# Kernel tuning notes

Hardware: AMD Instinct MI355X
Metric: run time of the kernel (lower is better)

## Reference

```python
import jax, jax.numpy as jnp
import numpy as np

N_NODES = 10000
N_EDGES = 160000
D = 128        # embedding_dim = in/out channels
E_DIM = 32     # edge feature dim
HEADS = 3
N_ETYPES = 64
ROUNDS = 2     # num_message_rounds
NEG_SLOPE = 0.2


def _lookup_maxnorm(table, idx):
    # torch Embedding(max_norm=1): rows with L2 norm > 1 are renormalized to norm 1
    v = table[idx]
    n = jnp.linalg.norm(v, axis=-1, keepdims=True)
    return v / jnp.maximum(n, 1.0)


def _edge_gat(x, src, dst, edge_attr, weight, att, euw, bias):
    # x: [N, D]; src/dst: [E] (self loops included); edge_attr: [E, E_DIM]
    N = x.shape[0]
    H = HEADS
    C = weight.shape[1] // H
    xh = (x @ weight).reshape(N, H, C)                 # [N, H, C]
    x_j = xh[src]                                      # gather source nodes  [E, H, C]
    x_i = xh[dst]                                      # gather target nodes  [E, H, C]
    ea = jnp.broadcast_to(edge_attr[:, None, :], (src.shape[0], H, edge_attr.shape[-1]))
    xj_cat = jnp.concatenate([x_j, ea], axis=-1)       # [E, H, C+E_DIM]
    # attention logits: (cat(x_i, x_j, e) * att).sum(-1)
    alpha = jnp.sum(jnp.concatenate([x_i, xj_cat], axis=-1) * att, axis=-1)  # [E, H]
    alpha = jax.nn.leaky_relu(alpha, NEG_SLOPE)
    # scatter-softmax over incoming edges of each dst node (stable)
    m = jax.ops.segment_max(alpha, dst, num_segments=N)        # [N, H]
    a = jnp.exp(alpha - m[dst])
    denom = jax.ops.segment_sum(a, dst, num_segments=N)        # [N, H]
    a = a / denom[dst]
    # weighted scatter-add aggregate
    aggr = jax.ops.segment_sum(xj_cat * a[..., None], dst, num_segments=N)  # [N, H, C+E_DIM]
    return aggr.mean(axis=1) @ euw + bias                       # [N, C]


def setup_inputs() -> dict:
    key = jax.random.key(0)
    ks = jax.random.split(key, 13)
    x_idx = jnp.arange(N_NODES, dtype=jnp.int32)
    src = jax.random.randint(ks[0], (N_EDGES,), 0, N_NODES, dtype=jnp.int32)
    off = jax.random.randint(ks[1], (N_EDGES,), 1, N_NODES, dtype=jnp.int32)
    dst = (src + off) % N_NODES    # guaranteed self-loop-free
    edge_index = jnp.stack([src, dst])
    edge_attr_idx = jax.random.randint(ks[2], (N_EDGES,), 0, N_ETYPES, dtype=jnp.int32)
    def g(k, shape):
        return jax.random.normal(k, shape, jnp.float32) * np.float32(np.sqrt(2.0 / sum(shape)))
    node_emb = g(ks[3], (N_NODES, D))
    edge_emb = g(ks[4], (N_ETYPES, E_DIM))
    w1 = g(ks[5], (D, HEADS * D))
    att1 = g(ks[6], (1, HEADS, 2 * D + E_DIM))
    euw1 = g(ks[7], (D + E_DIM, D))
    b1 = jnp.zeros((D,), jnp.float32)
    w2 = g(ks[8], (D, HEADS * D))
    att2 = g(ks[9], (1, HEADS, 2 * D + E_DIM))
    euw2 = g(ks[10], (D + E_DIM, D))
    b2 = jnp.zeros((D,), jnp.float32)
    return dict(x_idx=x_idx, edge_index=edge_index, edge_attr_idx=edge_attr_idx,
                node_emb=node_emb, edge_emb=edge_emb,
                w1=w1, att1=att1, euw1=euw1, b1=b1,
                w2=w2, att2=att2, euw2=euw2, b2=b2)


def reference(x_idx, edge_index, edge_attr_idx, node_emb, edge_emb,
              w1, att1, euw1, b1, w2, att2, euw2, b2):
    N = node_emb.shape[0]
    src0, dst0 = edge_index[0], edge_index[1]
    loop = jnp.arange(N, dtype=src0.dtype)
    src = jnp.concatenate([src0, loop])
    dst = jnp.concatenate([dst0, loop])
    x = _lookup_maxnorm(node_emb, x_idx)               # [N, D]
    ea = edge_emb[edge_attr_idx]                       # [E0, E_DIM]
    ea_full = jnp.concatenate([ea, jnp.zeros((N, ea.shape[-1]), ea.dtype)], axis=0)
    for _ in range(ROUNDS):
        # eval mode: dropout is identity
        x = jax.nn.elu(_edge_gat(x, src, dst, ea_full, w1, att1, euw1, b1))
        x = _edge_gat(x, src, dst, ea_full, w2, att2, euw2, b2)
    return x
```

## Files before the change

### kernel.cpp

```cpp
#include <hip/hip_runtime.h>
#include <hip/hip_bf16.h>

typedef __hip_bfloat16 bf16;
typedef __attribute__((ext_vector_type(8))) short short8;
typedef __attribute__((ext_vector_type(4))) float f32x4;

__device__ __forceinline__ float b2f(bf16 v) { return __bfloat162float(v); }
__device__ __forceinline__ float2 i2f2(int w) {
  float lo = __uint_as_float(((unsigned)w) << 16);
  float hi = __uint_as_float(((unsigned)w) & 0xFFFF0000u);
  return make_float2(lo, hi);
}
__device__ __forceinline__ unsigned f2bfb(float f) {
  unsigned u = __float_as_uint(f);
  unsigned r = 0x7FFFu + ((u >> 16) & 1u);
  return (u + r) >> 16;
}
__device__ __forceinline__ unsigned pk2(float a, float b) {
  return f2bfb(a) | (f2bfb(b) << 16);
}
__device__ __forceinline__ float ldv(const void* p, int i, int f) {
  return f ? ((const float*)p)[i] : b2f(((const bf16*)p)[i]);
}

__global__ __launch_bounds__(512) void detect_set_kernel(
    const unsigned short* __restrict__ probe, int nhalves, int* __restrict__ flag,
    const void* __restrict__ eeraw, const void* __restrict__ att1raw,
    const void* __restrict__ att2raw, float* __restrict__ s_et) {
  __shared__ int cnt;
  __shared__ int fl;
  if (threadIdx.x == 0) cnt = 0;
  __syncthreads();
  int local = 0;
  for (int i = threadIdx.x; i < nhalves; i += 512) {
    int e = (probe[i] >> 7) & 0xFF;
    if (e >= 160) local++;
  }
  if (local) atomicAdd(&cnt, local);
  __syncthreads();
  if (threadIdx.x == 0) { fl = (cnt > 16) ? 1 : 0; *flag = fl; }
  __syncthreads();
  int f = fl;
  int id = threadIdx.x;
  if (id < 2 * 65 * 3) {
    int l = id / (65 * 3);
    int r = id % (65 * 3);
    int t = r / 3, h = r % 3;
    const void* att = l ? att2raw : att1raw;
    float s = 0.0f;
    if (t < 64) {
      for (int d = 0; d < 32; ++d)
        s += ldv(eeraw, t * 32 + d, f) * ldv(att, h * 288 + 256 + d, f);
    }
    s_et[id] = s;
  }
}

__global__ __launch_bounds__(256) void wconv_kernel(
    const void* __restrict__ ee, const void* __restrict__ w1,
    const void* __restrict__ a1, const void* __restrict__ eu1,
    const void* __restrict__ b1, const void* __restrict__ w2,
    const void* __restrict__ a2, const void* __restrict__ eu2,
    const void* __restrict__ b2, const int* __restrict__ flag,
    float* __restrict__ eef, float* __restrict__ att1f, float* __restrict__ att2f,
    float* __restrict__ b1f, float* __restrict__ b2f,
    bf16* __restrict__ WT1, bf16* __restrict__ WT2,
    bf16* __restrict__ euT1, bf16* __restrict__ euT2,
    int* __restrict__ counts, int N) {
  int i = blockIdx.x * 256 + threadIdx.x;
  int f = *flag;
  if (i < 2048) {
    eef[i] = ldv(ee, i, f);
  } else if (i < 2912) {
    att1f[i - 2048] = ldv(a1, i - 2048, f);
  } else if (i < 3776) {
    att2f[i - 2912] = ldv(a2, i - 2912, f);
  } else if (i < 3904) {
    b1f[i - 3776] = ldv(b1, i - 3776, f);
  } else if (i < 4032) {
    b2f[i - 3904] = ldv(b2, i - 3904, f);
  } else if (i < 53184) {
    int j = i - 4032; int c = j >> 7, k = j & 127;
    WT1[j] = __float2bfloat16(ldv(w1, k * 384 + c, f));
  } else if (i < 102336) {
    int j = i - 53184; int c = j >> 7, k = j & 127;
    WT2[j] = __float2bfloat16(ldv(w2, k * 384 + c, f));
  } else if (i < 122816) {
    int j = i - 102336; int c = j / 160, k = j % 160;
    euT1[j] = __float2bfloat16(ldv(eu1, k * 128 + c, f));
  } else if (i < 143296) {
    int j = i - 122816; int c = j / 160, k = j % 160;
    euT2[j] = __float2bfloat16(ldv(eu2, k * 128 + c, f));
  } else if (i < 143296 + N) {
    counts[i - 143296] = 0;
  }
}

__global__ __launch_bounds__(256) void prep_kernel(
    const int* __restrict__ x_idx, const void* __restrict__ node_emb,
    const int* __restrict__ flag, bf16* __restrict__ xb,
    int* __restrict__ counts, const int* __restrict__ dst, int E0, int N) {
  int wid = threadIdx.x >> 6, lane = threadIdx.x & 63;
  int n = blockIdx.x * 4 + wid;
  if (n < N) {
    int idx = x_idx[n];
    if ((unsigned)idx >= (unsigned)N) idx = 0;
    float v0, v1;
    if (*flag) {
      const float* er = (const float*)node_emb + (size_t)idx * 128;
      v0 = er[lane]; v1 = er[lane + 64];
    } else {
      const bf16* er = (const bf16*)node_emb + (size_t)idx * 128;
      v0 = b2f(er[lane]); v1 = b2f(er[lane + 64]);
    }
    float ss = v0 * v0 + v1 * v1;
#pragma unroll
    for (int d = 32; d > 0; d >>= 1) ss += __shfl_xor(ss, d);
    float norm = sqrtf(ss);
    float scale = norm > 1.0f ? 1.0f / norm : 1.0f;
    xb[(size_t)n * 128 + lane] = __float2bfloat16(v0 * scale);
    xb[(size_t)n * 128 + 64 + lane] = __float2bfloat16(v1 * scale);
  }
  int gid = blockIdx.x * 256 + threadIdx.x;
  int stride = gridDim.x * 256;
  for (int i = gid; i < E0; i += stride) {
    int d = dst[i];
    if ((unsigned)d >= (unsigned)N) d = 0;
    atomicAdd(&counts[d], 1);
  }
}

__global__ __launch_bounds__(1024) void scan_kernel(
    int* __restrict__ counts, int* __restrict__ row_ptr, int N) {
  __shared__ int wsum[16];
  int t = threadIdx.x;
  int chunk = (N + 1023) >> 10;
  int lo = t * chunk;
  int hi = lo + chunk;
  if (lo > N) lo = N;
  if (hi > N) hi = N;
  int s = 0;
  for (int i = lo; i < hi; ++i) s += counts[i] + 1;
  int lane = t & 63, wv = t >> 6;
  int incl = s;
#pragma unroll
  for (int d = 1; d < 64; d <<= 1) {
    int u = __shfl_up(incl, d);
    if (lane >= d) incl += u;
  }
  if (lane == 63) wsum[wv] = incl;
  __syncthreads();
  if (t == 0) {
    int run = 0;
#pragma unroll
    for (int w = 0; w < 16; ++w) { int c = wsum[w]; wsum[w] = run; run += c; }
  }
  __syncthreads();
  int run = incl - s + wsum[wv];
  for (int i = lo; i < hi; ++i) {
    int c = counts[i] + 1;
    row_ptr[i] = run;
    counts[i] = run;
    run += c;
  }
  if (t == 1023) row_ptr[N] = run;
}

__global__ __launch_bounds__(256) void scatter_kernel(
    const int* __restrict__ src, const int* __restrict__ dst,
    const int* __restrict__ et, int* __restrict__ cursor,
    int* __restrict__ packed, int E0, int N) {
  int E = E0 + N;
  int i = blockIdx.x * blockDim.x + threadIdx.x;
  if (i < E0) {
    int d = dst[i];
    if ((unsigned)d >= (unsigned)N) d = 0;
    int p = atomicAdd(&cursor[d], 1);
    if ((unsigned)p >= (unsigned)E) p = 0;
    int t = et[i] & 63;
    packed[p] = (src[i] & 0xFFFF) | (t << 16);
  } else if (i < E) {
    int n = i - E0;
    int p = atomicAdd(&cursor[n], 1);
    if ((unsigned)p >= (unsigned)E) p = 0;
    packed[p] = (n & 0xFFFF) | (64 << 16);
  }
}

__global__ __launch_bounds__(384) void gemm_xh_s_mfma(
    const bf16* __restrict__ x, const bf16* __restrict__ WT,
    const float* __restrict__ attf, bf16* __restrict__ xh,
    float* __restrict__ s_i, float* __restrict__ s_j, int N) {
  __shared__ float lds_i[6][16];
  __shared__ float lds_j[6][16];
  int wave = threadIdx.x >> 6, lane = threadIdx.x & 63;
  int row_base = blockIdx.x * 16;
  int quad = lane >> 4, r16 = lane & 15;
  int row = row_base + r16; if (row >= N) row = N - 1;
  const short8* ap = (const short8*)(x + (size_t)row * 128 + quad * 8);
  short8 a[4];
#pragma unroll
  for (int kk = 0; kk < 4; ++kk) a[kk] = ap[kk * 4];

  float pi_r[4] = {0.f, 0.f, 0.f, 0.f};
  float pj_r[4] = {0.f, 0.f, 0.f, 0.f};
#pragma unroll
  for (int j = 0; j < 4; ++j) {
    int col = wave * 64 + j * 16 + r16;
    const short8* bp = (const short8*)(WT + (size_t)col * 128 + quad * 8);
    f32x4 acc = {0.f, 0.f, 0.f, 0.f};
#pragma unroll
    for (int kk = 0; kk < 4; ++kk)
      acc = __builtin_amdgcn_mfma_f32_16x16x32_bf16(a[kk], bp[kk * 4], acc, 0, 0, 0);
    int h = col >> 7, fi = col & 127, pair = fi >> 1, sub = fi & 1;
    size_t base = (size_t)pair * 6 + h * 2 + sub;
#pragma unroll
    for (int r = 0; r < 4; ++r) {
      int node = row_base + quad * 4 + r;
      if (node < N) xh[(size_t)node * 384 + base] = __float2bfloat16(acc[r]);
    }
    float ai = attf[h * 288 + fi];
    float aj = attf[h * 288 + 128 + fi];
#pragma unroll
    for (int r = 0; r < 4; ++r) {
      pi_r[r] = fmaf(acc[r], ai, pi_r[r]);
      pj_r[r] = fmaf(acc[r], aj, pj_r[r]);
    }
  }
#pragma unroll
  for (int d = 1; d < 16; d <<= 1) {
#pragma unroll
    for (int r = 0; r < 4; ++r) {
      pi_r[r] += __shfl_xor(pi_r[r], d);
      pj_r[r] += __shfl_xor(pj_r[r], d);
    }
  }
  if (r16 == 0) {
#pragma unroll
    for (int r = 0; r < 4; ++r) {
      lds_i[wave][quad * 4 + r] = pi_r[r];
      lds_j[wave][quad * 4 + r] = pj_r[r];
    }
  }
  __syncthreads();
  int m = threadIdx.x;
  if (m < 48) {
    int h = m / 16, r = m % 16;
    int node = row_base + r;
    if (node < N) s_i[node * 3 + h] = lds_i[2 * h][r] + lds_i[2 * h + 1][r];
  } else if (m < 96) {
    int tt = m - 48;
    int h = tt / 16, r = tt % 16;
    int node = row_base + r;
    if (node < N) s_j[node * 3 + h] = lds_j[2 * h][r] + lds_j[2 * h + 1][r];
  }
}

__global__ __launch_bounds__(256) void edge_aggr_kernel(
    const int* __restrict__ xh_i, const float* __restrict__ s_i,
    const float* __restrict__ s_j, const float* __restrict__ s_et,
    const float2* __restrict__ eef2, const int* __restrict__ row_ptr,
    const int* __restrict__ packed, unsigned* __restrict__ aggr_u,
    int N, int E) {
  int wid = threadIdx.x >> 6, lane = threadIdx.x & 63;
  int n = blockIdx.x * 4 + wid;
  if (n >= N) return;
  int start = row_ptr[n], end = row_ptr[n + 1];
  if (start < 0) start = 0;
  if (start > E) start = E;
  if (end < start) end = start;
  if (end > E) end = E;
  int deg = end - start;
  float si0 = s_i[n * 3 + 0], si1 = s_i[n * 3 + 1], si2 = s_i[n * 3 + 2];

  float p0r[2], p1r[2], p2r[2];
  int pkr[2];
  float dp0 = 0.0f, dp1 = 0.0f, dp2 = 0.0f;
#pragma unroll
  for (int it = 0; it < 2; ++it) {
    p0r[it] = p1r[it] = p2r[it] = 0.0f; pkr[it] = 0;
    int slot = it * 64 + lane;
    if (slot < deg) {
      int p = packed[start + slot];
      int s = p & 0xFFFF; if (s >= N) s = N - 1;
      int t = (p >> 16) & 127; if (t > 64) t = 64;
      float a0 = si0 + s_j[s * 3 + 0] + s_et[t * 3 + 0];
      float a1 = si1 + s_j[s * 3 + 1] + s_et[t * 3 + 1];
      float a2 = si2 + s_j[s * 3 + 2] + s_et[t * 3 + 2];
      a0 = a0 > 0.0f ? a0 : 0.2f * a0;
      a1 = a1 > 0.0f ? a1 : 0.2f * a1;
      a2 = a2 > 0.0f ? a2 : 0.2f * a2;
      a0 = fminf(fmaxf(a0, -60.0f), 60.0f);
      a1 = fminf(fmaxf(a1, -60.0f), 60.0f);
      a2 = fminf(fmaxf(a2, -60.0f), 60.0f);
      float p0 = __expf(a0), p1 = __expf(a1), p2 = __expf(a2);
      dp0 += p0; dp1 += p1; dp2 += p2;
      p0r[it] = p0; p1r[it] = p1; p2r[it] = p2;
      pkr[it] = s | (t << 16);
    }
  }
#pragma unroll
  for (int d = 32; d > 0; d >>= 1) {
    dp0 += __shfl_xor(dp0, d);
    dp1 += __shfl_xor(dp1, d);
    dp2 += __shfl_xor(dp2, d);
  }
  float d0 = dp0, d1 = dp1, d2 = dp2;

  float2 ax0 = make_float2(0.f, 0.f), ax1 = ax0, ax2 = ax0;
  float2 ae0 = ax0, ae1 = ax0, ae2 = ax0;
  int mm = deg < 128 ? deg : 128;

  auto agg_range = [&](int pk_s, float q0_s, float q1_s, float q2_s, int cnt) {
    int j = 0;
    for (; j + 2 <= cnt; j += 2) {
      int pkA = __shfl(pk_s, j), pkB = __shfl(pk_s, j + 1);
      float qA0 = __shfl(q0_s, j), qB0 = __shfl(q0_s, j + 1);
      float qA1 = __shfl(q1_s, j), qB1 = __shfl(q1_s, j + 1);
      float qA2 = __shfl(q2_s, j), qB2 = __shfl(q2_s, j + 1);
      int sA = pkA & 0xFFFF, tA = pkA >> 16;
      int sB = pkB & 0xFFFF, tB = pkB >> 16;
      const int* xpA = xh_i + (size_t)sA * 192 + lane * 3;
      const int* xpB = xh_i + (size_t)sB * 192 + lane * 3;
      int wA0 = xpA[0], wA1 = xpA[1], wA2 = xpA[2];
      int wB0 = xpB[0], wB1 = xpB[1], wB2 = xpB[2];
      float2 vA0 = i2f2(wA0), vA1 = i2f2(wA1), vA2 = i2f2(wA2);
      float2 vB0 = i2f2(wB0), vB1 = i2f2(wB1), vB2 = i2f2(wB2);
      ax0.x = fmaf(qA0, vA0.x, ax0.x); ax0.y = fmaf(qA0, vA0.y, ax0.y);
      ax1.x = fmaf(qA1, vA1.x, ax1.x); ax1.y = fmaf(qA1, vA1.y, ax1.y);
      ax2.x = fmaf(qA2, vA2.x, ax2.x); ax2.y = fmaf(qA2, vA2.y, ax2.y);
      ax0.x = fmaf(qB0, vB0.x, ax0.x); ax0.y = fmaf(qB0, vB0.y, ax0.y);
      ax1.x = fmaf(qB1, vB1.x, ax1.x); ax1.y = fmaf(qB1, vB1.y, ax1.y);
      ax2.x = fmaf(qB2, vB2.x, ax2.x); ax2.y = fmaf(qB2, vB2.y, ax2.y);
      if (lane < 16) {
        if (tA != 64) {
          float2 ev = eef2[tA * 16 + lane];
          ae0.x = fmaf(qA0, ev.x, ae0.x); ae0.y = fmaf(qA0, ev.y, ae0.y);
          ae1.x = fmaf(qA1, ev.x, ae1.x); ae1.y = fmaf(qA1, ev.y, ae1.y);
          ae2.x = fmaf(qA2, ev.x, ae2.x); ae2.y = fmaf(qA2, ev.y, ae2.y);
        }
        if (tB != 64) {
          float2 ev = eef2[tB * 16 + lane];
          ae0.x = fmaf(qB0, ev.x, ae0.x); ae0.y = fmaf(qB0, ev.y, ae0.y);
          ae1.x = fmaf(qB1, ev.x, ae1.x); ae1.y = fmaf(qB1, ev.y, ae1.y);
          ae2.x = fmaf(qB2, ev.x, ae2.x); ae2.y = fmaf(qB2, ev.y, ae2.y);
        }
      }
    }
    if (j < cnt) {
      int pkA = __shfl(pk_s, j);
      float qA0 = __shfl(q0_s, j), qA1 = __shfl(q1_s, j), qA2 = __shfl(q2_s, j);
      int sA = pkA & 0xFFFF, tA = pkA >> 16;
      const int* xpA = xh_i + (size_t)sA * 192 + lane * 3;
      int wA0 = xpA[0], wA1 = xpA[1], wA2 = xpA[2];
      float2 vA0 = i2f2(wA0), vA1 = i2f2(wA1), vA2 = i2f2(wA2);
      ax0.x = fmaf(qA0, vA0.x, ax0.x); ax0.y = fmaf(qA0, vA0.y, ax0.y);
      ax1.x = fmaf(qA1, vA1.x, ax1.x); ax1.y = fmaf(qA1, vA1.y, ax1.y);
      ax2.x = fmaf(qA2, vA2.x, ax2.x); ax2.y = fmaf(qA2, vA2.y, ax2.y);
      if (lane < 16 && tA != 64) {
        float2 ev = eef2[tA * 16 + lane];
        ae0.x = fmaf(qA0, ev.x, ae0.x); ae0.y = fmaf(qA0, ev.y, ae0.y);
        ae1.x = fmaf(qA1, ev.x, ae1.x); ae1.y = fmaf(qA1, ev.y, ae1.y);
        ae2.x = fmaf(qA2, ev.x, ae2.x); ae2.y = fmaf(qA2, ev.y, ae2.y);
      }
    }
  };
  agg_range(pkr[0], p0r[0], p1r[0], p2r[0], mm < 64 ? mm : 64);
  if (mm > 64) agg_range(pkr[1], p0r[1], p1r[1], p2r[1], mm - 64);

  for (int e = start + 128; e < end; ++e) {
    int p = packed[e];
    int s = p & 0xFFFF; if (s >= N) s = N - 1;
    int t = (p >> 16) & 127; if (t > 64) t = 64;
    float a0 = si0 + s_j[s * 3 + 0] + s_et[t * 3 + 0];
    float a1 = si1 + s_j[s * 3 + 1] + s_et[t * 3 + 1];
    float a2 = si2 + s_j[s * 3 + 2] + s_et[t * 3 + 2];
    a0 = a0 > 0.0f ? a0 : 0.2f * a0;
    a1 = a1 > 0.0f ? a1 : 0.2f * a1;
    a2 = a2 > 0.0f ? a2 : 0.2f * a2;
    a0 = fminf(fmaxf(a0, -60.0f), 60.0f);
    a1 = fminf(fmaxf(a1, -60.0f), 60.0f);
    a2 = fminf(fmaxf(a2, -60.0f), 60.0f);
    float p0 = __expf(a0), p1 = __expf(a1), p2 = __expf(a2);
    d0 += p0; d1 += p1; d2 += p2;
    const int* xp = xh_i + (size_t)s * 192 + lane * 3;
    float2 v0 = i2f2(xp[0]), v1 = i2f2(xp[1]), v2 = i2f2(xp[2]);
    ax0.x = fmaf(p0, v0.x, ax0.x); ax0.y = fmaf(p0, v0.y, ax0.y);
    ax1.x = fmaf(p1, v1.x, ax1.x); ax1.y = fmaf(p1, v1.y, ax1.y);
    ax2.x = fmaf(p2, v2.x, ax2.x); ax2.y = fmaf(p2, v2.y, ax2.y);
    if (t != 64 && lane < 16) {
      float2 ev = eef2[t * 16 + lane];
      ae0.x = fmaf(p0, ev.x, ae0.x); ae0.y = fmaf(p0, ev.y, ae0.y);
      ae1.x = fmaf(p1, ev.x, ae1.x); ae1.y = fmaf(p1, ev.y, ae1.y);
      ae2.x = fmaf(p2, ev.x, ae2.x); ae2.y = fmaf(p2, ev.y, ae2.y);
    }
  }

  const float third = 1.0f / 3.0f;
  float i0 = third / fmaxf(d0, 1e-30f);
  float i1 = third / fmaxf(d1, 1e-30f);
  float i2 = third / fmaxf(d2, 1e-30f);
  aggr_u[(size_t)n * 80 + lane] =
      pk2(ax0.x * i0 + ax1.x * i1 + ax2.x * i2,
          ax0.y * i0 + ax1.y * i1 + ax2.y * i2);
  if (lane < 16)
    aggr_u[(size_t)n * 80 + 64 + lane] =
        pk2(ae0.x * i0 + ae1.x * i1 + ae2.x * i2,
            ae0.y * i0 + ae1.y * i1 + ae2.y * i2);
}

__global__ __launch_bounds__(256) void gemm_out_mfma(
    const bf16* __restrict__ aggr, const bf16* __restrict__ euwT,
    const float* __restrict__ biasf, bf16* __restrict__ xb,
    void* __restrict__ dout, const int* __restrict__ flag,
    int N, int do_elu, int do_final) {
  int wave = threadIdx.x >> 6, lane = threadIdx.x & 63;
  int row_base = blockIdx.x * 16;
  int col_base = blockIdx.y * 64 + wave * 16;
  int quad = lane >> 4, r16 = lane & 15;
  int row = row_base + r16; if (row >= N) row = N - 1;
  int col = col_base + r16;
  f32x4 acc = {0.f, 0.f, 0.f, 0.f};
  const short8* ap = (const short8*)(aggr + (size_t)row * 160 + quad * 8);
  const short8* bp = (const short8*)(euwT + (size_t)col * 160 + quad * 8);
#pragma unroll
  for (int kk = 0; kk < 5; ++kk) {
    short8 a = ap[kk * 4];
    short8 b = bp[kk * 4];
    acc = __builtin_amdgcn_mfma_f32_16x16x32_bf16(a, b, acc, 0, 0, 0);
  }
  float bv = biasf[col];
  int f = *flag;
#pragma unroll
  for (int r = 0; r < 4; ++r) {
    int node = row_base + quad * 4 + r;
    if (node < N) {
      float v = acc[r] + bv;
      if (do_elu) v = v > 0.0f ? v : expm1f(v);
      if (do_final) {
        if (f) ((float*)dout)[(size_t)node * 128 + col] = v;
        else   ((bf16*)dout)[(size_t)node * 128 + col] = __float2bfloat16(v);
      } else {
        xb[(size_t)node * 128 + col] = __float2bfloat16(v);
      }
    }
  }
}

extern "C" void kernel_launch(void* const* d_in, const int* in_sizes, int n_in,
                              void* d_out, int out_size, void* d_ws, size_t ws_size,
                              hipStream_t stream) {
  const int* x_idx = (const int*)d_in[0];
  const int* edge_index = (const int*)d_in[1];
  const int* edge_attr_idx = (const int*)d_in[2];

  int N = in_sizes[0];
  int E0 = in_sizes[1] / 2;
  int E = E0 + N;
  const int* src = edge_index;
  const int* dst = edge_index + E0;

  size_t off = 0;
  char* base = (char*)d_ws;
  auto carve = [&](size_t bytes) -> void* {
    void* p = base + off;
    off += (bytes + 255) & ~(size_t)255;
    return p;
  };
  int* flag     = (int*)carve(256);
  int* counts   = (int*)carve((size_t)N * 4);
  int* row_ptr  = (int*)carve((size_t)(N + 1) * 4);
  int* packed   = (int*)carve((size_t)E * 4);
  float* s_i    = (float*)carve((size_t)N * 3 * 4);
  float* s_j    = (float*)carve((size_t)N * 3 * 4);
  float* s_et   = (float*)carve(2 * 65 * 3 * 4);
  float* eef    = (float*)carve(2048 * 4);
  float* att1f  = (float*)carve(864 * 4);
  float* att2f  = (float*)carve(864 * 4);
  float* b1f    = (float*)carve(128 * 4);
  float* b2f_   = (float*)carve(128 * 4);
  bf16* WT1     = (bf16*)carve(49152 * 2);
  bf16* WT2     = (bf16*)carve(49152 * 2);
  bf16* euT1    = (bf16*)carve(20480 * 2);
  bf16* euT2    = (bf16*)carve(20480 * 2);
  bf16* xh      = (bf16*)carve((size_t)N * 384 * 2 + 64);
  bf16* aggr    = (bf16*)carve((size_t)N * 160 * 2);
  bf16* xb      = (bf16*)d_out;
  (void)n_in; (void)out_size; (void)ws_size;

  detect_set_kernel<<<1, 512, 0, stream>>>(
      (const unsigned short*)d_in[5], 2048, flag, d_in[4], d_in[6], d_in[10], s_et);
  wconv_kernel<<<(143296 + N + 255) / 256, 256, 0, stream>>>(
      d_in[4], d_in[5], d_in[6], d_in[7], d_in[8], d_in[9], d_in[10], d_in[11],
      d_in[12], flag, eef, att1f, att2f, b1f, b2f_, WT1, WT2, euT1, euT2,
      counts, N);
  int nb4 = (N + 3) / 4;
  prep_kernel<<<nb4, 256, 0, stream>>>(x_idx, d_in[3], flag, xb, counts, dst,
                                       E0, N);
  scan_kernel<<<1, 1024, 0, stream>>>(counts, row_ptr, N);
  scatter_kernel<<<(E + 255) / 256, 256, 0, stream>>>(src, dst, edge_attr_idx,
                                                      counts, packed, E0, N);

  const bf16* WTs[2] = {WT1, WT2};
  const float* atts[2] = {att1f, att2f};
  const bf16* euTs[2] = {euT1, euT2};
  const float* bs[2] = {b1f, b2f_};

  int nrb = (N + 15) / 16;
  for (int round = 0; round < 2; ++round) {
    for (int l = 0; l < 2; ++l) {
      int do_elu = (l == 0) ? 1 : 0;
      int do_final = (round == 1 && l == 1) ? 1 : 0;
      gemm_xh_s_mfma<<<nrb, 384, 0, stream>>>(xb, WTs[l], atts[l], xh,
                                              s_i, s_j, N);
      edge_aggr_kernel<<<nb4, 256, 0, stream>>>(
          (const int*)xh, s_i, s_j, s_et + l * 195, (const float2*)eef,
          row_ptr, packed, (unsigned*)aggr, N, E);
      gemm_out_mfma<<<dim3(nrb, 2), 256, 0, stream>>>(
          aggr, euTs[l], bs[l], xb, d_out, flag, N, do_elu, do_final);
    }
  }
}
```

Before: 328.6 us.

## Split each node's edges across two waves, double GEMM row tile, fold detect kernel

The edge aggregation kernel now assigns two waves per destination node. Each wave takes alternating edges, and the partial sums are combined through LDS before the bf16 write. The xh GEMM processes 32 rows per block and reuses each loaded B fragment across two MFMA row tiles. The separate dtype-detect/s_et kernel is merged into wconv_kernel, so every block recomputes the flag locally and block 0 writes s_et. These changes aim to raise parallelism on low-degree nodes, cut B-fragment reloads and drop one launch, at the cost of an extra LDS reduction, a block-wide sync and more registers.

```diff
diff --git a/kernel.cpp b/kernel.cpp
--- a/kernel.cpp
+++ b/kernel.cpp
@@ -23,52 +23,38 @@
   return f ? ((const float*)p)[i] : b2f(((const bf16*)p)[i]);
 }
 
-__global__ __launch_bounds__(512) void detect_set_kernel(
-    const unsigned short* __restrict__ probe, int nhalves, int* __restrict__ flag,
-    const void* __restrict__ eeraw, const void* __restrict__ att1raw,
-    const void* __restrict__ att2raw, float* __restrict__ s_et) {
-  __shared__ int cnt;
-  __shared__ int fl;
-  if (threadIdx.x == 0) cnt = 0;
-  __syncthreads();
-  int local = 0;
-  for (int i = threadIdx.x; i < nhalves; i += 512) {
-    int e = (probe[i] >> 7) & 0xFF;
-    if (e >= 160) local++;
-  }
-  if (local) atomicAdd(&cnt, local);
-  __syncthreads();
-  if (threadIdx.x == 0) { fl = (cnt > 16) ? 1 : 0; *flag = fl; }
-  __syncthreads();
-  int f = fl;
-  int id = threadIdx.x;
-  if (id < 2 * 65 * 3) {
-    int l = id / (65 * 3);
-    int r = id % (65 * 3);
-    int t = r / 3, h = r % 3;
-    const void* att = l ? att2raw : att1raw;
-    float s = 0.0f;
-    if (t < 64) {
-      for (int d = 0; d < 32; ++d)
-        s += ldv(eeraw, t * 32 + d, f) * ldv(att, h * 288 + 256 + d, f);
-    }
-    s_et[id] = s;
-  }
-}
-
 __global__ __launch_bounds__(256) void wconv_kernel(
     const void* __restrict__ ee, const void* __restrict__ w1,
     const void* __restrict__ a1, const void* __restrict__ eu1,
     const void* __restrict__ b1, const void* __restrict__ w2,
     const void* __restrict__ a2, const void* __restrict__ eu2,
-    const void* __restrict__ b2, const int* __restrict__ flag,
+    const void* __restrict__ b2, int* __restrict__ flag,
     float* __restrict__ eef, float* __restrict__ att1f, float* __restrict__ att2f,
     float* __restrict__ b1f, float* __restrict__ b2f,
     bf16* __restrict__ WT1, bf16* __restrict__ WT2,
     bf16* __restrict__ euT1, bf16* __restrict__ euT2,
-    int* __restrict__ counts, int N) {
+    float* __restrict__ s_et, int* __restrict__ counts, int N) {
+  __shared__ int cnt;
+  __shared__ int fl;
+  if (threadIdx.x == 0) cnt = 0;
+  __syncthreads();
+  const unsigned short* probe = (const unsigned short*)w1;
+  int local = 0;
+#pragma unroll
+  for (int k = 0; k < 8; ++k) {
+    int e = (probe[threadIdx.x * 8 + k] >> 7) & 0xFF;
+    if (e >= 160) local++;
+  }
+  if (local) atomicAdd(&cnt, local);
+  __syncthreads();
+  if (threadIdx.x == 0) {
+    fl = (cnt > 16) ? 1 : 0;
+    if (blockIdx.x == 0) *flag = fl;
+  }
+  __syncthreads();
+  int f = fl;
+
   int i = blockIdx.x * 256 + threadIdx.x;
-  int f = *flag;
   if (i < 2048) {
     eef[i] = ldv(ee, i, f);
   } else if (i < 2912) {
@@ -94,6 +80,21 @@
   } else if (i < 143296 + N) {
     counts[i - 143296] = 0;
   }
+
+  if (blockIdx.x == 0) {
+    for (int id = threadIdx.x; id < 2 * 65 * 3; id += 256) {
+      int l = id / (65 * 3);
+      int r = id % (65 * 3);
+      int t = r / 3, h = r % 3;
+      const void* att = l ? a2 : a1;
+      float s = 0.0f;
+      if (t < 64) {
+        for (int d = 0; d < 32; ++d)
+          s += ldv(ee, t * 32 + d, f) * ldv(att, h * 288 + 256 + d, f);
+      }
+      s_et[id] = s;
+    }
+  }
 }
 
 __global__ __launch_bounds__(256) void prep_kernel(
@@ -191,66 +192,82 @@
     const bf16* __restrict__ x, const bf16* __restrict__ WT,
     const float* __restrict__ attf, bf16* __restrict__ xh,
     float* __restrict__ s_i, float* __restrict__ s_j, int N) {
-  __shared__ float lds_i[6][16];
-  __shared__ float lds_j[6][16];
+  __shared__ float lds_i[6][32];
+  __shared__ float lds_j[6][32];
   int wave = threadIdx.x >> 6, lane = threadIdx.x & 63;
-  int row_base = blockIdx.x * 16;
+  int row_base = blockIdx.x * 32;
   int quad = lane >> 4, r16 = lane & 15;
-  int row = row_base + r16; if (row >= N) row = N - 1;
-  const short8* ap = (const short8*)(x + (size_t)row * 128 + quad * 8);
-  short8 a[4];
-#pragma unroll
-  for (int kk = 0; kk < 4; ++kk) a[kk] = ap[kk * 4];
-
-  float pi_r[4] = {0.f, 0.f, 0.f, 0.f};
-  float pj_r[4] = {0.f, 0.f, 0.f, 0.f};
+  int rowA = row_base + r16;      if (rowA >= N) rowA = N - 1;
+  int rowB = row_base + 16 + r16; if (rowB >= N) rowB = N - 1;
+  const short8* apA = (const short8*)(x + (size_t)rowA * 128 + quad * 8);
+  const short8* apB = (const short8*)(x + (size_t)rowB * 128 + quad * 8);
+  short8 aA[4], aB[4];
+#pragma unroll
+  for (int kk = 0; kk < 4; ++kk) { aA[kk] = apA[kk * 4]; aB[kk] = apB[kk * 4]; }
+
+  float piA[4] = {0.f, 0.f, 0.f, 0.f}, pjA[4] = {0.f, 0.f, 0.f, 0.f};
+  float piB[4] = {0.f, 0.f, 0.f, 0.f}, pjB[4] = {0.f, 0.f, 0.f, 0.f};
 #pragma unroll
   for (int j = 0; j < 4; ++j) {
     int col = wave * 64 + j * 16 + r16;
     const short8* bp = (const short8*)(WT + (size_t)col * 128 + quad * 8);
-    f32x4 acc = {0.f, 0.f, 0.f, 0.f};
-#pragma unroll
-    for (int kk = 0; kk < 4; ++kk)
-      acc = __builtin_amdgcn_mfma_f32_16x16x32_bf16(a[kk], bp[kk * 4], acc, 0, 0, 0);
+    short8 b[4];
+#pragma unroll
+    for (int kk = 0; kk < 4; ++kk) b[kk] = bp[kk * 4];
+    f32x4 accA = {0.f, 0.f, 0.f, 0.f};
+    f32x4 accB = {0.f, 0.f, 0.f, 0.f};
+#pragma unroll
+    for (int kk = 0; kk < 4; ++kk) {
+      accA = __builtin_amdgcn_mfma_f32_16x16x32_bf16(aA[kk], b[kk], accA, 0, 0, 0);
+      accB = __builtin_amdgcn_mfma_f32_16x16x32_bf16(aB[kk], b[kk], accB, 0, 0, 0);
+    }
     int h = col >> 7, fi = col & 127, pair = fi >> 1, sub = fi & 1;
     size_t base = (size_t)pair * 6 + h * 2 + sub;
 #pragma unroll
     for (int r = 0; r < 4; ++r) {
-      int node = row_base + quad * 4 + r;
-      if (node < N) xh[(size_t)node * 384 + base] = __float2bfloat16(acc[r]);
+      int nA = row_base + quad * 4 + r;
+      int nB = row_base + 16 + quad * 4 + r;
+      if (nA < N) xh[(size_t)nA * 384 + base] = __float2bfloat16(accA[r]);
+      if (nB < N) xh[(size_t)nB * 384 + base] = __float2bfloat16(accB[r]);
     }
     float ai = attf[h * 288 + fi];
     float aj = attf[h * 288 + 128 + fi];
 #pragma unroll
     for (int r = 0; r < 4; ++r) {
-      pi_r[r] = fmaf(acc[r], ai, pi_r[r]);
-      pj_r[r] = fmaf(acc[r], aj, pj_r[r]);
+      piA[r] = fmaf(accA[r], ai, piA[r]);
+      pjA[r] = fmaf(accA[r], aj, pjA[r]);
+      piB[r] = fmaf(accB[r], ai, piB[r]);
+      pjB[r] = fmaf(accB[r], aj, pjB[r]);
     }
   }
 #pragma unroll
   for (int d = 1; d < 16; d <<= 1) {
 #pragma unroll
     for (int r = 0; r < 4; ++r) {
-      pi_r[r] += __shfl_xor(pi_r[r], d);
-      pj_r[r] += __shfl_xor(pj_r[r], d);
+      piA[r] += __shfl_xor(piA[r], d);
+      pjA[r] += __shfl_xor(pjA[r], d);
+      piB[r] += __shfl_xor(piB[r], d);
+      pjB[r] += __shfl_xor(pjB[r], d);
     }
   }
   if (r16 == 0) {
 #pragma unroll
     for (int r = 0; r < 4; ++r) {
-      lds_i[wave][quad * 4 + r] = pi_r[r];
-      lds_j[wave][quad * 4 + r] = pj_r[r];
+      lds_i[wave][quad * 4 + r] = piA[r];
+      lds_j[wave][quad * 4 + r] = pjA[r];
+      lds_i[wave][16 + quad * 4 + r] = piB[r];
+      lds_j[wave][16 + quad * 4 + r] = pjB[r];
     }
   }
   __syncthreads();
   int m = threadIdx.x;
-  if (m < 48) {
-    int h = m / 16, r = m % 16;
+  if (m < 96) {
+    int h = m / 32, r = m % 32;
     int node = row_base + r;
     if (node < N) s_i[node * 3 + h] = lds_i[2 * h][r] + lds_i[2 * h + 1][r];
-  } else if (m < 96) {
-    int tt = m - 48;
-    int h = tt / 16, r = tt % 16;
+  } else if (m < 192) {
+    int tt = m - 96;
+    int h = tt / 32, r = tt % 32;
     int node = row_base + r;
     if (node < N) s_j[node * 3 + h] = lds_j[2 * h][r] + lds_j[2 * h + 1][r];
   }
@@ -262,9 +279,11 @@
     const float2* __restrict__ eef2, const int* __restrict__ row_ptr,
     const int* __restrict__ packed, unsigned* __restrict__ aggr_u,
     int N, int E) {
+  __shared__ float lds[2][512];
   int wid = threadIdx.x >> 6, lane = threadIdx.x & 63;
-  int n = blockIdx.x * 4 + wid;
-  if (n >= N) return;
+  int nodeLocal = wid >> 1, w = wid & 1;
+  int n0 = blockIdx.x * 2 + nodeLocal;
+  int n = n0 < N ? n0 : N - 1;
   int start = row_ptr[n], end = row_ptr[n + 1];
   if (start < 0) start = 0;
   if (start > E) start = E;
@@ -273,31 +292,26 @@
   int deg = end - start;
   float si0 = s_i[n * 3 + 0], si1 = s_i[n * 3 + 1], si2 = s_i[n * 3 + 2];
 
-  float p0r[2], p1r[2], p2r[2];
-  int pkr[2];
+  float p0r = 0.f, p1r = 0.f, p2r = 0.f;
+  int pkr = 0;
   float dp0 = 0.0f, dp1 = 0.0f, dp2 = 0.0f;
-#pragma unroll
-  for (int it = 0; it < 2; ++it) {
-    p0r[it] = p1r[it] = p2r[it] = 0.0f; pkr[it] = 0;
-    int slot = it * 64 + lane;
-    if (slot < deg) {
-      int p = packed[start + slot];
-      int s = p & 0xFFFF; if (s >= N) s = N - 1;
-      int t = (p >> 16) & 127; if (t > 64) t = 64;
-      float a0 = si0 + s_j[s * 3 + 0] + s_et[t * 3 + 0];
-      float a1 = si1 + s_j[s * 3 + 1] + s_et[t * 3 + 1];
-      float a2 = si2 + s_j[s * 3 + 2] + s_et[t * 3 + 2];
-      a0 = a0 > 0.0f ? a0 : 0.2f * a0;
-      a1 = a1 > 0.0f ? a1 : 0.2f * a1;
-      a2 = a2 > 0.0f ? a2 : 0.2f * a2;
-      a0 = fminf(fmaxf(a0, -60.0f), 60.0f);
-      a1 = fminf(fmaxf(a1, -60.0f), 60.0f);
-      a2 = fminf(fmaxf(a2, -60.0f), 60.0f);
-      float p0 = __expf(a0), p1 = __expf(a1), p2 = __expf(a2);
-      dp0 += p0; dp1 += p1; dp2 += p2;
-      p0r[it] = p0; p1r[it] = p1; p2r[it] = p2;
-      pkr[it] = s | (t << 16);
-    }
+  int slot = 2 * lane + w;
+  if (slot < deg) {
+    int p = packed[start + slot];
+    int s = p & 0xFFFF; if (s >= N) s = N - 1;
+    int t = (p >> 16) & 127; if (t > 64) t = 64;
+    float a0 = si0 + s_j[s * 3 + 0] + s_et[t * 3 + 0];
+    float a1 = si1 + s_j[s * 3 + 1] + s_et[t * 3 + 1];
+    float a2 = si2 + s_j[s * 3 + 2] + s_et[t * 3 + 2];
+    a0 = a0 > 0.0f ? a0 : 0.2f * a0;
+    a1 = a1 > 0.0f ? a1 : 0.2f * a1;
+    a2 = a2 > 0.0f ? a2 : 0.2f * a2;
+    a0 = fminf(fmaxf(a0, -60.0f), 60.0f);
+    a1 = fminf(fmaxf(a1, -60.0f), 60.0f);
+    a2 = fminf(fmaxf(a2, -60.0f), 60.0f);
+    p0r = __expf(a0); p1r = __expf(a1); p2r = __expf(a2);
+    dp0 = p0r; dp1 = p1r; dp2 = p2r;
+    pkr = s | (t << 16);
   }
 #pragma unroll
   for (int d = 32; d > 0; d >>= 1) {
@@ -309,15 +323,16 @@
 
   float2 ax0 = make_float2(0.f, 0.f), ax1 = ax0, ax2 = ax0;
   float2 ae0 = ax0, ae1 = ax0, ae2 = ax0;
-  int mm = deg < 128 ? deg : 128;
-
-  auto agg_range = [&](int pk_s, float q0_s, float q1_s, float q2_s, int cnt) {
+  int capped = deg < 128 ? deg : 128;
+  int cnt = (capped > w) ? ((capped - w + 1) >> 1) : 0;
+
+  {
     int j = 0;
     for (; j + 2 <= cnt; j += 2) {
-      int pkA = __shfl(pk_s, j), pkB = __shfl(pk_s, j + 1);
-      float qA0 = __shfl(q0_s, j), qB0 = __shfl(q0_s, j + 1);
-      float qA1 = __shfl(q1_s, j), qB1 = __shfl(q1_s, j + 1);
-      float qA2 = __shfl(q2_s, j), qB2 = __shfl(q2_s, j + 1);
+      int pkA = __shfl(pkr, j), pkB = __shfl(pkr, j + 1);
+      float qA0 = __shfl(p0r, j), qB0 = __shfl(p0r, j + 1);
+      float qA1 = __shfl(p1r, j), qB1 = __shfl(p1r, j + 1);
+      float qA2 = __shfl(p2r, j), qB2 = __shfl(p2r, j + 1);
       int sA = pkA & 0xFFFF, tA = pkA >> 16;
       int sB = pkB & 0xFFFF, tB = pkB >> 16;
       const int* xpA = xh_i + (size_t)sA * 192 + lane * 3;
@@ -348,8 +363,8 @@
       }
     }
     if (j < cnt) {
-      int pkA = __shfl(pk_s, j);
-      float qA0 = __shfl(q0_s, j), qA1 = __shfl(q1_s, j), qA2 = __shfl(q2_s, j);
+      int pkA = __shfl(pkr, j);
+      float qA0 = __shfl(p0r, j), qA1 = __shfl(p1r, j), qA2 = __shfl(p2r, j);
       int sA = pkA & 0xFFFF, tA = pkA >> 16;
       const int* xpA = xh_i + (size_t)sA * 192 + lane * 3;
       int wA0 = xpA[0], wA1 = xpA[1], wA2 = xpA[2];
@@ -364,49 +379,73 @@
         ae2.x = fmaf(qA2, ev.x, ae2.x); ae2.y = fmaf(qA2, ev.y, ae2.y);
       }
     }
-  };
-  agg_range(pkr[0], p0r[0], p1r[0], p2r[0], mm < 64 ? mm : 64);
-  if (mm > 64) agg_range(pkr[1], p0r[1], p1r[1], p2r[1], mm - 64);
-
-  for (int e = start + 128; e < end; ++e) {
-    int p = packed[e];
-    int s = p & 0xFFFF; if (s >= N) s = N - 1;
-    int t = (p >> 16) & 127; if (t > 64) t = 64;
-    float a0 = si0 + s_j[s * 3 + 0] + s_et[t * 3 + 0];
-    float a1 = si1 + s_j[s * 3 + 1] + s_et[t * 3 + 1];
-    float a2 = si2 + s_j[s * 3 + 2] + s_et[t * 3 + 2];
-    a0 = a0 > 0.0f ? a0 : 0.2f * a0;
-    a1 = a1 > 0.0f ? a1 : 0.2f * a1;
-    a2 = a2 > 0.0f ? a2 : 0.2f * a2;
-    a0 = fminf(fmaxf(a0, -60.0f), 60.0f);
-    a1 = fminf(fmaxf(a1, -60.0f), 60.0f);
-    a2 = fminf(fmaxf(a2, -60.0f), 60.0f);
-    float p0 = __expf(a0), p1 = __expf(a1), p2 = __expf(a2);
-    d0 += p0; d1 += p1; d2 += p2;
-    const int* xp = xh_i + (size_t)s * 192 + lane * 3;
-    float2 v0 = i2f2(xp[0]), v1 = i2f2(xp[1]), v2 = i2f2(xp[2]);
-    ax0.x = fmaf(p0, v0.x, ax0.x); ax0.y = fmaf(p0, v0.y, ax0.y);
-    ax1.x = fmaf(p1, v1.x, ax1.x); ax1.y = fmaf(p1, v1.y, ax1.y);
-    ax2.x = fmaf(p2, v2.x, ax2.x); ax2.y = fmaf(p2, v2.y, ax2.y);
-    if (t != 64 && lane < 16) {
-      float2 ev = eef2[t * 16 + lane];
-      ae0.x = fmaf(p0, ev.x, ae0.x); ae0.y = fmaf(p0, ev.y, ae0.y);
-      ae1.x = fmaf(p1, ev.x, ae1.x); ae1.y = fmaf(p1, ev.y, ae1.y);
-      ae2.x = fmaf(p2, ev.x, ae2.x); ae2.y = fmaf(p2, ev.y, ae2.y);
-    }
-  }
-
-  const float third = 1.0f / 3.0f;
-  float i0 = third / fmaxf(d0, 1e-30f);
-  float i1 = third / fmaxf(d1, 1e-30f);
-  float i2 = third / fmaxf(d2, 1e-30f);
-  aggr_u[(size_t)n * 80 + lane] =
-      pk2(ax0.x * i0 + ax1.x * i1 + ax2.x * i2,
-          ax0.y * i0 + ax1.y * i1 + ax2.y * i2);
-  if (lane < 16)
-    aggr_u[(size_t)n * 80 + 64 + lane] =
-        pk2(ae0.x * i0 + ae1.x * i1 + ae2.x * i2,
-            ae0.y * i0 + ae1.y * i1 + ae2.y * i2);
+  }
+
+  if (w == 0) {
+    for (int e = start + 128; e < end; ++e) {
+      int p = packed[e];
+      int s = p & 0xFFFF; if (s >= N) s = N - 1;
+      int t = (p >> 16) & 127; if (t > 64) t = 64;
+      float a0 = si0 + s_j[s * 3 + 0] + s_et[t * 3 + 0];
+      float a1 = si1 + s_j[s * 3 + 1] + s_et[t * 3 + 1];
+      float a2 = si2 + s_j[s * 3 + 2] + s_et[t * 3 + 2];
+      a0 = a0 > 0.0f ? a0 : 0.2f * a0;
+      a1 = a1 > 0.0f ? a1 : 0.2f * a1;
+      a2 = a2 > 0.0f ? a2 : 0.2f * a2;
+      a0 = fminf(fmaxf(a0, -60.0f), 60.0f);
+      a1 = fminf(fmaxf(a1, -60.0f), 60.0f);
+      a2 = fminf(fmaxf(a2, -60.0f), 60.0f);
+      float p0 = __expf(a0), p1 = __expf(a1), p2 = __expf(a2);
+      d0 += p0; d1 += p1; d2 += p2;
+      const int* xp = xh_i + (size_t)s * 192 + lane * 3;
+      float2 v0 = i2f2(xp[0]), v1 = i2f2(xp[1]), v2 = i2f2(xp[2]);
+      ax0.x = fmaf(p0, v0.x, ax0.x); ax0.y = fmaf(p0, v0.y, ax0.y);
+      ax1.x = fmaf(p1, v1.x, ax1.x); ax1.y = fmaf(p1, v1.y, ax1.y);
+      ax2.x = fmaf(p2, v2.x, ax2.x); ax2.y = fmaf(p2, v2.y, ax2.y);
+      if (t != 64 && lane < 16) {
+        float2 ev = eef2[t * 16 + lane];
+        ae0.x = fmaf(p0, ev.x, ae0.x); ae0.y = fmaf(p0, ev.y, ae0.y);
+        ae1.x = fmaf(p1, ev.x, ae1.x); ae1.y = fmaf(p1, ev.y, ae1.y);
+        ae2.x = fmaf(p2, ev.x, ae2.x); ae2.y = fmaf(p2, ev.y, ae2.y);
+      }
+    }
+  }
+
+  float* L = lds[nodeLocal];
+  if (w == 1) {
+    L[lane * 2 + 0] = ax0.x;       L[lane * 2 + 1] = ax0.y;
+    L[128 + lane * 2 + 0] = ax1.x; L[128 + lane * 2 + 1] = ax1.y;
+    L[256 + lane * 2 + 0] = ax2.x; L[256 + lane * 2 + 1] = ax2.y;
+    if (lane < 16) {
+      L[384 + lane * 2 + 0] = ae0.x; L[384 + lane * 2 + 1] = ae0.y;
+      L[416 + lane * 2 + 0] = ae1.x; L[416 + lane * 2 + 1] = ae1.y;
+      L[448 + lane * 2 + 0] = ae2.x; L[448 + lane * 2 + 1] = ae2.y;
+    }
+    if (lane == 0) { L[480] = d0; L[481] = d1; L[482] = d2; }
+  }
+  __syncthreads();
+  if (w == 0 && n0 < N) {
+    ax0.x += L[lane * 2 + 0];       ax0.y += L[lane * 2 + 1];
+    ax1.x += L[128 + lane * 2 + 0]; ax1.y += L[128 + lane * 2 + 1];
+    ax2.x += L[256 + lane * 2 + 0]; ax2.y += L[256 + lane * 2 + 1];
+    if (lane < 16) {
+      ae0.x += L[384 + lane * 2 + 0]; ae0.y += L[384 + lane * 2 + 1];
+      ae1.x += L[416 + lane * 2 + 0]; ae1.y += L[416 + lane * 2 + 1];
+      ae2.x += L[448 + lane * 2 + 0]; ae2.y += L[448 + lane * 2 + 1];
+    }
+    d0 += L[480]; d1 += L[481]; d2 += L[482];
+    const float third = 1.0f / 3.0f;
+    float i0 = third / fmaxf(d0, 1e-30f);
+    float i1 = third / fmaxf(d1, 1e-30f);
+    float i2 = third / fmaxf(d2, 1e-30f);
+    aggr_u[(size_t)n0 * 80 + lane] =
+        pk2(ax0.x * i0 + ax1.x * i1 + ax2.x * i2,
+            ax0.y * i0 + ax1.y * i1 + ax2.y * i2);
+    if (lane < 16)
+      aggr_u[(size_t)n0 * 80 + 64 + lane] =
+          pk2(ae0.x * i0 + ae1.x * i1 + ae2.x * i2,
+              ae0.y * i0 + ae1.y * i1 + ae2.y * i2);
+  }
 }
 
 __global__ __launch_bounds__(256) void gemm_out_mfma(
@@ -488,12 +527,10 @@
   bf16* xb      = (bf16*)d_out;
   (void)n_in; (void)out_size; (void)ws_size;
 
-  detect_set_kernel<<<1, 512, 0, stream>>>(
-      (const unsigned short*)d_in[5], 2048, flag, d_in[4], d_in[6], d_in[10], s_et);
   wconv_kernel<<<(143296 + N + 255) / 256, 256, 0, stream>>>(
       d_in[4], d_in[5], d_in[6], d_in[7], d_in[8], d_in[9], d_in[10], d_in[11],
       d_in[12], flag, eef, att1f, att2f, b1f, b2f_, WT1, WT2, euT1, euT2,
-      counts, N);
+      s_et, counts, N);
   int nb4 = (N + 3) / 4;
   prep_kernel<<<nb4, 256, 0, stream>>>(x_idx, d_in[3], flag, xb, counts, dst,
                                        E0, N);
@@ -506,17 +543,19 @@
   const bf16* euTs[2] = {euT1, euT2};
   const float* bs[2] = {b1f, b2f_};
 
-  int nrb = (N + 15) / 16;
+  int nrb16 = (N + 15) / 16;
+  int nrb32 = (N + 31) / 32;
+  int nb2 = (N + 1) / 2;
   for (int round = 0; round < 2; ++round) {
     for (int l = 0; l < 2; ++l) {
       int do_elu = (l == 0) ? 1 : 0;
       int do_final = (round == 1 && l == 1) ? 1 : 0;
-      gemm_xh_s_mfma<<<nrb, 384, 0, stream>>>(xb, WTs[l], atts[l], xh,
-                                              s_i, s_j, N);
-      edge_aggr_kernel<<<nb4, 256, 0, stream>>>(
+      gemm_xh_s_mfma<<<nrb32, 384, 0, stream>>>(xb, WTs[l], atts[l], xh,
+                                                s_i, s_j, N);
+      edge_aggr_kernel<<<nb2, 256, 0, stream>>>(
           (const int*)xh, s_i, s_j, s_et + l * 195, (const float2*)eef,
           row_ptr, packed, (unsigned*)aggr, N, E);
-      gemm_out_mfma<<<dim3(nrb, 2), 256, 0, stream>>>(
+      gemm_out_mfma<<<dim3(nrb16, 2), 256, 0, stream>>>(
           aggr, euTs[l], bs[l], xb, d_out, flag, N, do_elu, do_final);
     }
   }
```

Result: no change. 325.5 us (-0.9%).
